# Performance work log

Hardware: AMD Instinct MI355X
Metric: run time of the kernel (lower is better)

Reference implementation:

```python
import jax, jax.numpy as jnp
import numpy as np

D_MODEL = 768
NUM_HEADS = 12
D_K = D_MODEL // NUM_HEADS
BATCH = 1
SEQ = 4096


def setup_inputs() -> dict:
    key = jax.random.key(0)
    ks = jax.random.split(key, 11)
    s = 0.02
    inp = {
        'Q': jax.random.normal(ks[0], (BATCH, SEQ, D_MODEL), jnp.float32),
        'K': jax.random.normal(ks[1], (BATCH, SEQ, D_MODEL), jnp.float32),
        'V': jax.random.normal(ks[2], (BATCH, SEQ, D_MODEL), jnp.float32),
        'Wq': jax.random.normal(ks[3], (D_MODEL, D_MODEL), jnp.float32) * s,
        'bq': jnp.zeros((D_MODEL,), jnp.float32),
        'Wk': jax.random.normal(ks[4], (D_MODEL, D_MODEL), jnp.float32) * s,
        'bk': jnp.zeros((D_MODEL,), jnp.float32),
        'Wv': jax.random.normal(ks[5], (D_MODEL, D_MODEL), jnp.float32) * s,
        'bv': jnp.zeros((D_MODEL,), jnp.float32),
        'Wo': jax.random.normal(ks[6], (D_MODEL, D_MODEL), jnp.float32) * s,
        'bo': jnp.zeros((D_MODEL,), jnp.float32),
    }
    return inp


def reference(Q, K, V, Wq, bq, Wk, bk, Wv, bv, Wo, bo):
    B, S, _ = Q.shape
    # Linear projections (torch Linear: x @ W^T + b)
    q = Q @ Wq.T + bq
    k = K @ Wk.T + bk
    v = V @ Wv.T + bv
    # split heads: (B, S, D) -> (B, H, S, d_k)
    def split(x):
        return x.reshape(B, S, NUM_HEADS, D_K).transpose(0, 2, 1, 3)
    q, k, v = split(q), split(k), split(v)
    # scaled dot-product attention (dropout = identity in eval)
    scores = jnp.einsum('bhqd,bhkd->bhqk', q, k) / jnp.sqrt(jnp.float32(D_K))
    attn_weights = jax.nn.softmax(scores, axis=-1)
    ctx = jnp.einsum('bhqk,bhkd->bhqd', attn_weights, v)
    # merge heads and output projection
    ctx = ctx.transpose(0, 2, 1, 3).reshape(B, S, D_MODEL)
    output = ctx @ Wo.T + bo
    return (output, attn_weights)
```

## Files before the change

kernel.cpp:

```cpp
#include <hip/hip_runtime.h>
#include <hip/hip_bf16.h>

#define S 4096
#define DM 768
#define NH 12
#define DK 64
#define KSPLIT 4
#define KHALF (S / KSPLIT)
#define RPARTS 8
#define RCHUNK (S / RPARTS)

typedef __bf16 bf16x8 __attribute__((ext_vector_type(8)));
typedef __bf16 bf16x4 __attribute__((ext_vector_type(4)));
typedef float f32x4 __attribute__((ext_vector_type(4)));
using bf16 = __hip_bfloat16;

__device__ inline bf16x8 load_frag(const bf16* p) {
    return *reinterpret_cast<const bf16x8*>(p);
}

__global__ void k_detect(const unsigned int* __restrict__ q, int* __restrict__ flag) {
    const int lane = threadIdx.x;
    int cnt = 0;
    for (int i = lane; i < 1024; i += 64) {
        const unsigned int w = q[i];
        const int e = (w >> 7) & 0xFF;
        if (e >= 192 || (e > 0 && e < 64)) cnt++;
    }
    for (int m = 1; m < 64; m <<= 1) cnt += __shfl_xor(cnt, m, 64);
    if (lane == 0) flag[0] = (cnt > 64) ? 1 : 0;
}

__device__ inline void cast_body(const void* src, bf16* dst, int n, int isf32) {
    const int stride = gridDim.x * 256 * 8;
    for (int i = (blockIdx.x * 256 + threadIdx.x) * 8; i < n; i += stride) {
        if (isf32) {
            const float* s = (const float*)src + i;
            float4 a = *(const float4*)(s);
            float4 b = *(const float4*)(s + 4);
            bf16x8 o;
            o[0] = (__bf16)a.x; o[1] = (__bf16)a.y; o[2] = (__bf16)a.z; o[3] = (__bf16)a.w;
            o[4] = (__bf16)b.x; o[5] = (__bf16)b.y; o[6] = (__bf16)b.z; o[7] = (__bf16)b.w;
            *reinterpret_cast<bf16x8*>(dst + i) = o;
        } else {
            *reinterpret_cast<bf16x8*>(dst + i) =
                *reinterpret_cast<const bf16x8*>((const __bf16*)src + i);
        }
    }
}

__global__ __launch_bounds__(256) void k_cast3(
    const void* s0, const void* s1, const void* s2,
    bf16* d0, bf16* d1, bf16* d2, int n, const int* __restrict__ flag) {
    const int t = blockIdx.y;
    const void* s = (t == 0) ? s0 : (t == 1) ? s1 : s2;
    bf16* d = (t == 0) ? d0 : (t == 1) ? d1 : d2;
    cast_body(s, d, n, flag[0]);
}

__global__ __launch_bounds__(256) void k_cast4(
    const void* s0, const void* s1, const void* s2, const void* s3,
    bf16* d0, bf16* d1, bf16* d2, bf16* d3, int n, const int* __restrict__ flag) {
    const int t = blockIdx.y;
    const void* s = (t == 0) ? s0 : (t == 1) ? s1 : (t == 2) ? s2 : s3;
    bf16* d = (t == 0) ? d0 : (t == 1) ? d1 : (t == 2) ? d2 : d3;
    cast_body(s, d, n, flag[0]);
}

__device__ inline void proj_body(
    const bf16* __restrict__ X, const bf16* __restrict__ W,
    const bf16* __restrict__ bias, void* __restrict__ dstv, int mode, int isf32)
{
    const int lane = threadIdx.x & 63;
    const int w    = threadIdx.x >> 6;
    const int lr   = lane & 15, lg = lane >> 4;
    const int rbase = blockIdx.x * 64 + w * 16;
    const int nbase = blockIdx.y * 64;

    f32x4 acc[4] = {};
    const bf16* xrow = X + (size_t)(rbase + lr) * DM + lg * 8;
    for (int kk = 0; kk < DM; kk += 32) {
        bf16x8 a = load_frag(xrow + kk);
#pragma unroll
        for (int nt = 0; nt < 4; ++nt) {
            bf16x8 b = load_frag(W + (size_t)(nbase + nt * 16 + lr) * DM + kk + lg * 8);
            acc[nt] = __builtin_amdgcn_mfma_f32_16x16x32_bf16(a, b, acc[nt], 0, 0, 0);
        }
    }
#pragma unroll
    for (int nt = 0; nt < 4; ++nt) {
        const int col = nbase + nt * 16 + lr;
        const float bv = __bfloat162float(bias[col]);
#pragma unroll
        for (int r = 0; r < 4; ++r) {
            const int row = rbase + lg * 4 + r;
            const float v = acc[nt][r] + bv;
            if (mode == 3) {
                const size_t off = (size_t)row * DM + col;
                if (isf32) ((float*)dstv)[off] = v;
                else       ((bf16*)dstv)[off] = __float2bfloat16(v);
            } else {
                size_t off;
                if (mode == 2) off = (size_t)col * S + row;
                else           off = (size_t)(col >> 6) * (S * DK) + (size_t)row * DK + (col & 63);
                ((bf16*)dstv)[off] = __float2bfloat16(v);
            }
        }
    }
}

__global__ __launch_bounds__(256) void k_proj_qkv(
    const bf16* __restrict__ Qc, const bf16* __restrict__ Kc, const bf16* __restrict__ Vc,
    const bf16* __restrict__ Wq, const bf16* __restrict__ Wk, const bf16* __restrict__ Wv,
    const bf16* __restrict__ bq, const bf16* __restrict__ bk, const bf16* __restrict__ bv,
    bf16* __restrict__ qh, bf16* __restrict__ kh, bf16* __restrict__ vt,
    const int* __restrict__ flag)
{
    const int z = blockIdx.z;
    const bf16* X = (z == 0) ? Qc : (z == 1) ? Kc : Vc;
    const bf16* W = (z == 0) ? Wq : (z == 1) ? Wk : Wv;
    const bf16* B = (z == 0) ? bq : (z == 1) ? bk : bv;
    bf16* D      = (z == 0) ? qh : (z == 1) ? kh : vt;
    proj_body(X, W, B, D, (z == 2) ? 2 : 0, flag[0]);
}

__global__ __launch_bounds__(256) void k_proj_out(
    const bf16* __restrict__ X, const bf16* __restrict__ W,
    const bf16* __restrict__ bias, void* __restrict__ dstv,
    const int* __restrict__ flag)
{
    proj_body(X, W, bias, dstv, 3, flag[0]);
}

__global__ __launch_bounds__(256) void k_rowsum(
    const bf16* __restrict__ qh, const bf16* __restrict__ kh,
    float* __restrict__ rs)
{
    const int lane = threadIdx.x & 63;
    const int w    = threadIdx.x >> 6;
    const int lr   = lane & 15;
    const int lg   = lane >> 4;
    const int h    = blockIdx.y;
    const int part = blockIdx.z;
    const int qw   = blockIdx.x * 256 + w * 64;

    const bf16* qb = qh + (size_t)h * (S * DK);
    const bf16* kb = kh + (size_t)h * (S * DK);
    bf16x8 aq[4][2];
#pragma unroll
    for (int qs = 0; qs < 4; ++qs) {
        aq[qs][0] = load_frag(qb + (size_t)(qw + qs * 16 + lr) * DK + lg * 8);
        aq[qs][1] = load_frag(qb + (size_t)(qw + qs * 16 + lr) * DK + 32 + lg * 8);
    }

    float s[4] = {0.f, 0.f, 0.f, 0.f};
    for (int kp = part * RCHUNK; kp < part * RCHUNK + RCHUNK; kp += 16) {
        bf16x8 b0 = load_frag(kb + (size_t)(kp + lr) * DK + lg * 8);
        bf16x8 b1 = load_frag(kb + (size_t)(kp + lr) * DK + 32 + lg * 8);
#pragma unroll
        for (int qs = 0; qs < 4; ++qs) {
            f32x4 d = {};
            d = __builtin_amdgcn_mfma_f32_16x16x32_bf16(b0, aq[qs][0], d, 0, 0, 0);
            d = __builtin_amdgcn_mfma_f32_16x16x32_bf16(b1, aq[qs][1], d, 0, 0, 0);
            s[qs] += __expf(d[0] * 0.125f) + __expf(d[1] * 0.125f) +
                     __expf(d[2] * 0.125f) + __expf(d[3] * 0.125f);
        }
    }
#pragma unroll
    for (int qs = 0; qs < 4; ++qs) {
        float v = s[qs];
        v += __shfl_xor(v, 16, 64);
        v += __shfl_xor(v, 32, 64);
        if (lg == 0)
            rs[((size_t)part * NH + h) * S + qw + qs * 16 + lr] = v;
    }
}

__global__ __launch_bounds__(256) void k_attn(
    const bf16* __restrict__ qh, const bf16* __restrict__ kh,
    const bf16* __restrict__ vt, const float* __restrict__ rs,
    void* __restrict__ doutv, float* __restrict__ ctxF,
    const int* __restrict__ flag)
{
    __shared__ __align__(16) bf16 Plds[4][2][16][136];
    const int isf32 = flag[0];
    const int lane = threadIdx.x & 63;
    const int w    = threadIdx.x >> 6;
    const int lr   = lane & 15, lg = lane >> 4;
    const int h    = blockIdx.y;
    const int half = blockIdx.z;
    const int q0w  = blockIdx.x * 128 + w * 32;
    const int k0   = half * KHALF;

    const bf16* qb = qh + (size_t)h * (S * DK);
    const bf16* kb = kh + (size_t)h * (S * DK);
    const bf16* vb = vt + (size_t)h * (S * DK);

    bf16x8 aq[2][2];
    float  inv[2];
#pragma unroll
    for (int qs = 0; qs < 2; ++qs) {
        const int qr = q0w + qs * 16 + lr;
        aq[qs][0] = load_frag(qb + (size_t)qr * DK + lg * 8);
        aq[qs][1] = load_frag(qb + (size_t)qr * DK + 32 + lg * 8);
        float ssum = 0.f;
#pragma unroll
        for (int p = 0; p < RPARTS; ++p)
            ssum += rs[((size_t)p * NH + h) * S + qr];
        inv[qs] = 1.0f / ssum;
    }

    float* poutF = (float*)doutv + (size_t)S * DM + (size_t)h * S * S;
    bf16*  poutB = (bf16*)doutv  + (size_t)S * DM + (size_t)h * S * S;

    const int fr2 = lane >> 5;
    const int fc2 = (lane & 31) * 4;

    f32x4 acc[2][4] = {};
    for (int tp = 0; tp < KHALF / 128; ++tp) {
#pragma unroll
        for (int tt = 0; tt < 2; ++tt) {
            const int kt = k0 + tp * 128 + tt * 64;
            const int cb = tt * 64;
            bf16x8 vv[4][2];
#pragma unroll
            for (int dt = 0; dt < 4; ++dt) {
                vv[dt][0] = load_frag(vb + (size_t)(dt * 16 + lr) * S + kt + lg * 8);
                vv[dt][1] = load_frag(vb + (size_t)(dt * 16 + lr) * S + kt + 32 + lg * 8);
            }
#pragma unroll
            for (int sub = 0; sub < 4; ++sub) {
                const int kp = kt + sub * 16;
                bf16x8 b0 = load_frag(kb + (size_t)(kp + lr) * DK + lg * 8);
                bf16x8 b1 = load_frag(kb + (size_t)(kp + lr) * DK + 32 + lg * 8);
#pragma unroll
                for (int qs = 0; qs < 2; ++qs) {
                    f32x4 d = {};
                    d = __builtin_amdgcn_mfma_f32_16x16x32_bf16(b0, aq[qs][0], d, 0, 0, 0);
                    d = __builtin_amdgcn_mfma_f32_16x16x32_bf16(b1, aq[qs][1], d, 0, 0, 0);
                    bf16x4 pv;
                    pv[0] = (__bf16)(__expf(d[0] * 0.125f) * inv[qs]);
                    pv[1] = (__bf16)(__expf(d[1] * 0.125f) * inv[qs]);
                    pv[2] = (__bf16)(__expf(d[2] * 0.125f) * inv[qs]);
                    pv[3] = (__bf16)(__expf(d[3] * 0.125f) * inv[qs]);
                    *reinterpret_cast<bf16x4*>(
                        &Plds[w][qs][lr][cb + sub * 16 + 4 * lg]) = pv;
                }
            }
            bf16x8 ap[2][2];
#pragma unroll
            for (int qs = 0; qs < 2; ++qs) {
                ap[qs][0] = *reinterpret_cast<const bf16x8*>(&Plds[w][qs][lr][cb + lg * 8]);
                ap[qs][1] = *reinterpret_cast<const bf16x8*>(&Plds[w][qs][lr][cb + 32 + lg * 8]);
            }
#pragma unroll
            for (int dt = 0; dt < 4; ++dt) {
#pragma unroll
                for (int qs = 0; qs < 2; ++qs) {
                    acc[qs][dt] = __builtin_amdgcn_mfma_f32_16x16x32_bf16(ap[qs][0], vv[dt][0], acc[qs][dt], 0, 0, 0);
                    acc[qs][dt] = __builtin_amdgcn_mfma_f32_16x16x32_bf16(ap[qs][1], vv[dt][1], acc[qs][dt], 0, 0, 0);
                }
            }
        }
        const int ktbase = k0 + tp * 128;
        if (isf32) {
#pragma unroll
            for (int j = 0; j < 16; ++j) {
                const int row = 2 * j + fr2;
                const int qs = row >> 4, rr = row & 15;
                bf16x4 x = *reinterpret_cast<const bf16x4*>(&Plds[w][qs][rr][fc2]);
                f32x4 o;
                o[0] = (float)x[0]; o[1] = (float)x[1];
                o[2] = (float)x[2]; o[3] = (float)x[3];
                __builtin_nontemporal_store(
                    o, reinterpret_cast<f32x4*>(
                           poutF + (size_t)(q0w + row) * S + ktbase + fc2));
            }
        } else {
#pragma unroll
            for (int j = 0; j < 16; ++j) {
                const int row = 2 * j + fr2;
                const int qs = row >> 4, rr = row & 15;
                bf16x4 x = *reinterpret_cast<const bf16x4*>(&Plds[w][qs][rr][fc2]);
                *reinterpret_cast<bf16x4*>(
                    poutB + (size_t)(q0w + row) * S + ktbase + fc2) = x;
            }
        }
    }
#pragma unroll
    for (int qs = 0; qs < 2; ++qs)
#pragma unroll
        for (int dt = 0; dt < 4; ++dt)
#pragma unroll
            for (int r = 0; r < 4; ++r)
                atomicAdd(&ctxF[(size_t)(q0w + qs * 16 + 4 * lg + r) * DM +
                                h * DK + dt * 16 + lr], acc[qs][dt][r]);
}

__global__ __launch_bounds__(256) void k_zero(float* __restrict__ p) {
    const int i = (blockIdx.x * 256 + threadIdx.x) * 4;
    f32x4 z = {};
    *reinterpret_cast<f32x4*>(p + i) = z;
}

__global__ __launch_bounds__(256) void k_reduce(const float* __restrict__ ctxF,
                                               bf16* __restrict__ ctx) {
    const int i = (blockIdx.x * 256 + threadIdx.x) * 8;
    f32x4 a = *reinterpret_cast<const f32x4*>(ctxF + i);
    f32x4 b = *reinterpret_cast<const f32x4*>(ctxF + i + 4);
    bf16x8 o;
#pragma unroll
    for (int j = 0; j < 4; ++j) o[j] = (__bf16)a[j];
#pragma unroll
    for (int j = 0; j < 4; ++j) o[4 + j] = (__bf16)b[j];
    *reinterpret_cast<bf16x8*>(ctx + i) = o;
}

extern "C" void kernel_launch(void* const* d_in, const int* in_sizes, int n_in,
                              void* d_out, int out_size, void* d_ws, size_t ws_size,
                              hipStream_t stream) {
    char* wsb = (char*)d_ws;
    int*   flag = (int*)wsb;
    float* rs   = (float*)(wsb + 16);
    bf16*  conv = (bf16*)(wsb + 16 + (size_t)RPARTS * NH * S * 4);

    const size_t nQ = (size_t)S * DM, nW = (size_t)DM * DM, nB = DM;
    bf16* Qc  = conv;
    bf16* Kc  = Qc + nQ;
    bf16* Vc  = Kc + nQ;
    bf16* Wqc = Vc + nQ;
    bf16* Wkc = Wqc + nW;
    bf16* Wvc = Wkc + nW;
    bf16* Woc = Wvc + nW;
    bf16* bqc = Woc + nW;
    bf16* bkc = bqc + nB;
    bf16* bvc = bkc + nB;
    bf16* boc = bvc + nB;
    bf16* qh  = boc + nB;
    bf16* kh  = qh + nQ;
    bf16* vt  = kh + nQ;
    float* ctxF = (float*)Qc;
    bf16*  ctx  = Vc;

    const size_t need = (size_t)((char*)(vt + nQ) - wsb);
    if (ws_size < need) return;

    dim3 blk(256);
    k_detect<<<1, 64, 0, stream>>>((const unsigned int*)d_in[0], flag);

    k_cast3<<<dim3((int)(nQ / 2048), 3), blk, 0, stream>>>(
        d_in[0], d_in[1], d_in[2], Qc, Kc, Vc, (int)nQ, flag);
    k_cast4<<<dim3((int)(nW / 2048), 4), blk, 0, stream>>>(
        d_in[3], d_in[5], d_in[7], d_in[9], Wqc, Wkc, Wvc, Woc, (int)nW, flag);
    k_cast4<<<dim3(1, 4), blk, 0, stream>>>(
        d_in[4], d_in[6], d_in[8], d_in[10], bqc, bkc, bvc, boc, (int)nB, flag);

    k_proj_qkv<<<dim3(S / 64, DM / 64, 3), blk, 0, stream>>>(
        Qc, Kc, Vc, Wqc, Wkc, Wvc, bqc, bkc, bvc, qh, kh, vt, flag);
    k_zero<<<dim3((int)(nQ / 1024)), blk, 0, stream>>>(ctxF);
    k_rowsum<<<dim3(S / 256, NH, RPARTS), blk, 0, stream>>>(qh, kh, rs);
    k_attn<<<dim3(S / 128, NH, KSPLIT), blk, 0, stream>>>(qh, kh, vt, rs, d_out, ctxF, flag);
    k_reduce<<<dim3((int)(nQ / 2048)), blk, 0, stream>>>(ctxF, ctx);
    k_proj_out<<<dim3(S / 64, DM / 64), blk, 0, stream>>>(ctx, Woc, boc, d_out, flag);
}
```

Before: 494.5 us.

## Replace atomic ctx accumulation with per-split bf16 partials summed in output projection

```diff
diff --git a/kernel.cpp b/kernel.cpp
--- a/kernel.cpp
+++ b/kernel.cpp
@@ -5,7 +5,7 @@
 #define DM 768
 #define NH 12
 #define DK 64
-#define KSPLIT 4
+#define KSPLIT 2
 #define KHALF (S / KSPLIT)
 #define RPARTS 8
 #define RCHUNK (S / RPARTS)
@@ -95,16 +95,10 @@
         for (int r = 0; r < 4; ++r) {
             const int row = rbase + lg * 4 + r;
             const float v = acc[nt][r] + bv;
-            if (mode == 3) {
-                const size_t off = (size_t)row * DM + col;
-                if (isf32) ((float*)dstv)[off] = v;
-                else       ((bf16*)dstv)[off] = __float2bfloat16(v);
-            } else {
-                size_t off;
-                if (mode == 2) off = (size_t)col * S + row;
-                else           off = (size_t)(col >> 6) * (S * DK) + (size_t)row * DK + (col & 63);
-                ((bf16*)dstv)[off] = __float2bfloat16(v);
-            }
+            size_t off;
+            if (mode == 2) off = (size_t)col * S + row;
+            else           off = (size_t)(col >> 6) * (S * DK) + (size_t)row * DK + (col & 63);
+            ((bf16*)dstv)[off] = __float2bfloat16(v);
         }
     }
 }
@@ -125,11 +119,46 @@
 }
 
 __global__ __launch_bounds__(256) void k_proj_out(
-    const bf16* __restrict__ X, const bf16* __restrict__ W,
+    const bf16* __restrict__ ctxp, const bf16* __restrict__ W,
     const bf16* __restrict__ bias, void* __restrict__ dstv,
     const int* __restrict__ flag)
 {
-    proj_body(X, W, bias, dstv, 3, flag[0]);
+    const int isf32 = flag[0];
+    const int lane = threadIdx.x & 63;
+    const int w    = threadIdx.x >> 6;
+    const int lr   = lane & 15, lg = lane >> 4;
+    const int rbase = blockIdx.x * 64 + w * 16;
+    const int nbase = blockIdx.y * 64;
+
+    f32x4 acc[4] = {};
+    const bf16* x0 = ctxp + (size_t)(rbase + lr) * DM + lg * 8;
+    const bf16* x1 = x0 + (size_t)S * DM;
+    for (int kk = 0; kk < DM; kk += 32) {
+        bf16x8 a0 = load_frag(x0 + kk);
+        bf16x8 a1 = load_frag(x1 + kk);
+        bf16x8 a;
+#pragma unroll
+        for (int j = 0; j < 8; ++j)
+            a[j] = (__bf16)((float)a0[j] + (float)a1[j]);
+#pragma unroll
+        for (int nt = 0; nt < 4; ++nt) {
+            bf16x8 b = load_frag(W + (size_t)(nbase + nt * 16 + lr) * DM + kk + lg * 8);
+            acc[nt] = __builtin_amdgcn_mfma_f32_16x16x32_bf16(a, b, acc[nt], 0, 0, 0);
+        }
+    }
+#pragma unroll
+    for (int nt = 0; nt < 4; ++nt) {
+        const int col = nbase + nt * 16 + lr;
+        const float bv = __bfloat162float(bias[col]);
+#pragma unroll
+        for (int r = 0; r < 4; ++r) {
+            const int row = rbase + lg * 4 + r;
+            const float v = acc[nt][r] + bv;
+            const size_t off = (size_t)row * DM + col;
+            if (isf32) ((float*)dstv)[off] = v;
+            else       ((bf16*)dstv)[off] = __float2bfloat16(v);
+        }
+    }
 }
 
 __global__ __launch_bounds__(256) void k_rowsum(
@@ -179,7 +208,7 @@
 __global__ __launch_bounds__(256) void k_attn(
     const bf16* __restrict__ qh, const bf16* __restrict__ kh,
     const bf16* __restrict__ vt, const float* __restrict__ rs,
-    void* __restrict__ doutv, float* __restrict__ ctxF,
+    void* __restrict__ doutv, bf16* __restrict__ ctxp,
     const int* __restrict__ flag)
 {
     __shared__ __align__(16) bf16 Plds[4][2][16][136];
@@ -287,33 +316,15 @@
             }
         }
     }
+    bf16* cp = ctxp + (size_t)half * S * DM;
 #pragma unroll
     for (int qs = 0; qs < 2; ++qs)
 #pragma unroll
         for (int dt = 0; dt < 4; ++dt)
 #pragma unroll
             for (int r = 0; r < 4; ++r)
-                atomicAdd(&ctxF[(size_t)(q0w + qs * 16 + 4 * lg + r) * DM +
-                                h * DK + dt * 16 + lr], acc[qs][dt][r]);
-}
-
-__global__ __launch_bounds__(256) void k_zero(float* __restrict__ p) {
-    const int i = (blockIdx.x * 256 + threadIdx.x) * 4;
-    f32x4 z = {};
-    *reinterpret_cast<f32x4*>(p + i) = z;
-}
-
-__global__ __launch_bounds__(256) void k_reduce(const float* __restrict__ ctxF,
-                                               bf16* __restrict__ ctx) {
-    const int i = (blockIdx.x * 256 + threadIdx.x) * 8;
-    f32x4 a = *reinterpret_cast<const f32x4*>(ctxF + i);
-    f32x4 b = *reinterpret_cast<const f32x4*>(ctxF + i + 4);
-    bf16x8 o;
-#pragma unroll
-    for (int j = 0; j < 4; ++j) o[j] = (__bf16)a[j];
-#pragma unroll
-    for (int j = 0; j < 4; ++j) o[4 + j] = (__bf16)b[j];
-    *reinterpret_cast<bf16x8*>(ctx + i) = o;
+                cp[(size_t)(q0w + qs * 16 + 4 * lg + r) * DM + h * DK + dt * 16 + lr] =
+                    __float2bfloat16(acc[qs][dt][r]);
 }
 
 extern "C" void kernel_launch(void* const* d_in, const int* in_sizes, int n_in,
@@ -339,8 +350,7 @@
     bf16* qh  = boc + nB;
     bf16* kh  = qh + nQ;
     bf16* vt  = kh + nQ;
-    float* ctxF = (float*)Qc;
-    bf16*  ctx  = Vc;
+    bf16* ctxp = Qc;
 
     const size_t need = (size_t)((char*)(vt + nQ) - wsb);
     if (ws_size < need) return;
@@ -357,9 +367,7 @@
 
     k_proj_qkv<<<dim3(S / 64, DM / 64, 3), blk, 0, stream>>>(
         Qc, Kc, Vc, Wqc, Wkc, Wvc, bqc, bkc, bvc, qh, kh, vt, flag);
-    k_zero<<<dim3((int)(nQ / 1024)), blk, 0, stream>>>(ctxF);
     k_rowsum<<<dim3(S / 256, NH, RPARTS), blk, 0, stream>>>(qh, kh, rs);
-    k_attn<<<dim3(S / 128, NH, KSPLIT), blk, 0, stream>>>(qh, kh, vt, rs, d_out, ctxF, flag);
-    k_reduce<<<dim3((int)(nQ / 2048)), blk, 0, stream>>>(ctxF, ctx);
-    k_proj_out<<<dim3(S / 64, DM / 64), blk, 0, stream>>>(ctx, Woc, boc, d_out, flag);
-}
+    k_attn<<<dim3(S / 128, NH, KSPLIT), blk, 0, stream>>>(qh, kh, vt, rs, d_out, ctxp, flag);
+    k_proj_out<<<dim3(S / 64, DM / 64), blk, 0, stream>>>(ctxp, Woc, boc, d_out, flag);
+}
```

Result: faster. 470.4 us (-4.9%).
